# Kernel optimization log

Measured on AMD Instinct MI355X. Metric: run time of the kernel, lower is better.

## Reference

```python
import jax, jax.numpy as jnp
import numpy as np

H_DIM = 64      # input_dim of edge_aggregation (== h_dim)
HID = 128       # hidden_size of each per-edge-type agg MLP
T = 5           # edge_types for non-nba dataset
B, E, N = 64, 1024, 512


def setup_inputs() -> dict:
    key = jax.random.key(0)
    ks = jax.random.split(key, 8)
    edge_distribution = jax.random.uniform(ks[0], (B, E, T), dtype=jnp.float32)
    H = jax.random.uniform(ks[1], (B, E, N), dtype=jnp.float32)
    ori = jax.random.normal(ks[2], (B, N, H_DIM), dtype=jnp.float32)
    s1 = 1.0 / np.sqrt(H_DIM)
    s2 = 1.0 / np.sqrt(HID)
    # stacked per-edge-type MLP params: Linear(64->128) -> ReLU -> Linear(128->64)
    W1 = jax.random.uniform(ks[3], (T, H_DIM, HID), minval=-s1, maxval=s1, dtype=jnp.float32)
    b1 = jax.random.uniform(ks[4], (T, HID), minval=-s1, maxval=s1, dtype=jnp.float32)
    W2 = jax.random.uniform(ks[5], (T, HID, H_DIM), minval=-s2, maxval=s2, dtype=jnp.float32)
    b2 = jax.random.uniform(ks[6], (T, H_DIM), minval=-s2, maxval=s2, dtype=jnp.float32)
    return {"edge_distribution": edge_distribution, "H": H, "ori": ori,
            "W1": W1, "b1": b1, "W2": W2, "b2": b2}


def reference(edge_distribution, H, ori, W1, b1, W2, b2):
    # incidence gather: hyperedge features [B, E, D]
    edges = jnp.matmul(H, ori)
    # per-edge-type 2-layer MLP, vectorized over the T edge types
    h = jax.nn.relu(jnp.einsum('bed,tdh->bteh', edges, W1) + b1[None, :, None, :])
    per_type = jnp.einsum('bteh,thd->bted', h, W2) + b2[None, :, None, :]
    # mixture-weighted sum over edge types -> [B, E, D]
    edge_feature = jnp.einsum('bet,bted->bed', edge_distribution, per_type)
    # scatter back through H^T and concat with original node features
    node_agg = jnp.einsum('ben,bed->bnd', H, edge_feature)  # H^T @ edge_feature
    node_feature = jnp.concatenate((node_agg, ori), axis=-1)  # [B, N, 2D]
    return node_feature
```

## Files before the change

### kernel.cpp

```cpp
#include <hip/hip_runtime.h>

#define B_   64
#define E_   1024
#define N_   512
#define D_   64
#define HID_ 128
#define T_   5

typedef __bf16 bf16x8 __attribute__((ext_vector_type(8)));
typedef float f32x4 __attribute__((ext_vector_type(4)));

__device__ __forceinline__ unsigned short f2bu(float f) {
    union { float f; unsigned int u; } v; v.f = f;
    unsigned int r = (v.u + 0x7fffu + ((v.u >> 16) & 1u)) >> 16;
    return (unsigned short)r;
}

#define MFMA16(a, b, c) __builtin_amdgcn_mfma_f32_16x16x32_bf16((a), (b), (c), 0, 0, 0)

__global__ __launch_bounds__(256) void k_prep_w(const float* __restrict__ W1,
                                                const float* __restrict__ W2,
                                                unsigned short* __restrict__ W1T,
                                                unsigned short* __restrict__ W2T) {
    int idx = blockIdx.x * 256 + threadIdx.x;
    if (idx < T_ * HID_ * D_) {
        int t = idx / (HID_ * D_), rem = idx % (HID_ * D_);
        int h = rem / D_, d = rem % D_;
        W1T[idx] = f2bu(W1[(t * D_ + d) * HID_ + h]);
    } else {
        int j = idx - T_ * HID_ * D_;
        int t = j / (D_ * HID_), rem = j % (D_ * HID_);
        int d = rem / HID_, h = rem % HID_;
        W2T[j] = f2bu(W2[(t * HID_ + h) * D_ + d]);
    }
}

__global__ __launch_bounds__(256) void k_ori_prep(const float* __restrict__ ori,
                                                  float* __restrict__ out,
                                                  unsigned short* __restrict__ oriT) {
    int b = blockIdx.y, n0 = blockIdx.x * 64;
    __shared__ float tl[64 * 65];
    int tid = threadIdx.x;
    int dl = tid & 63;
    #pragma unroll 4
    for (int p = 0; p < 16; ++p) {
        int nn = p * 4 + (tid >> 6);
        float v = ori[(size_t)(b * N_ + n0 + nn) * D_ + dl];
        out[(size_t)(b * N_ + n0 + nn) * 128 + 64 + dl] = v;
        tl[dl * 65 + nn] = v;
    }
    __syncthreads();
    #pragma unroll 4
    for (int p = 0; p < 16; ++p) {
        int dd = p * 4 + (tid >> 6);
        oriT[(size_t)(b * D_ + dd) * N_ + n0 + dl] = f2bu(tl[dd * 65 + dl]);
    }
}

__global__ __launch_bounds__(256) void k_gemm_edges(const float* __restrict__ H,
                                                    const unsigned short* __restrict__ oriT,
                                                    unsigned short* __restrict__ edges) {
    int b = blockIdx.y, e0 = blockIdx.x * 128;
    __shared__ __align__(16) unsigned short aA[128 * 40];
    __shared__ __align__(16) unsigned short bB[64 * 40];
    int tid = threadIdx.x, w = tid >> 6, l = tid & 63, q = l >> 4, c = l & 15;
    const f32x4 zero = {0.f, 0.f, 0.f, 0.f};
    f32x4 acc[2][4];
    #pragma unroll
    for (int fm = 0; fm < 2; ++fm)
        #pragma unroll
        for (int fn = 0; fn < 4; ++fn) acc[fm][fn] = zero;

    for (int ks = 0; ks < 16; ++ks) {
        int k0 = ks * 32;
        #pragma unroll
        for (int p = 0; p < 4; ++p) {
            int u = p * 256 + tid, r = u >> 3, sg = u & 7;
            const float4 f = *(const float4*)&H[(size_t)(b * E_ + e0 + r) * N_ + k0 + sg * 4];
            ushort4 o;
            o.x = f2bu(f.x); o.y = f2bu(f.y); o.z = f2bu(f.z); o.w = f2bu(f.w);
            *(ushort4*)&aA[r * 40 + sg * 4] = o;
        }
        {
            int dd = tid >> 2, sg = tid & 3;
            *(uint4*)&bB[dd * 40 + sg * 8] =
                *(const uint4*)&oriT[(size_t)(b * D_ + dd) * N_ + k0 + sg * 8];
        }
        __syncthreads();
        bf16x8 a0 = *(const bf16x8*)&aA[(w * 32 + c) * 40 + q * 8];
        bf16x8 a1 = *(const bf16x8*)&aA[(w * 32 + 16 + c) * 40 + q * 8];
        #pragma unroll
        for (int fn = 0; fn < 4; ++fn) {
            bf16x8 bb = *(const bf16x8*)&bB[(fn * 16 + c) * 40 + q * 8];
            acc[0][fn] = MFMA16(a0, bb, acc[0][fn]);
            acc[1][fn] = MFMA16(a1, bb, acc[1][fn]);
        }
        __syncthreads();
    }
    #pragma unroll
    for (int fm = 0; fm < 2; ++fm)
        #pragma unroll
        for (int fn = 0; fn < 4; ++fn)
            #pragma unroll
            for (int i = 0; i < 4; ++i) {
                int e = e0 + w * 32 + fm * 16 + q * 4 + i;
                int d = fn * 16 + c;
                edges[(size_t)(b * E_ + e) * D_ + d] = f2bu(acc[fm][fn][i]);
            }
}

__global__ __launch_bounds__(256) void k_mlp(const unsigned short* __restrict__ edges,
                                             const float* __restrict__ ed,
                                             const float* __restrict__ b1,
                                             const float* __restrict__ b2,
                                             const unsigned short* __restrict__ W1T,
                                             const unsigned short* __restrict__ W2T,
                                             unsigned short* __restrict__ efT) {
    int bx = blockIdx.x;
    int b = bx >> 4, e0 = (bx & 15) * 64;
    __shared__ __align__(16) unsigned short a_sh[64 * 72];
    __shared__ __align__(16) unsigned short w_sh[128 * 72];
    __shared__ __align__(16) unsigned short h_sh[64 * 136];
    __shared__ float wd_sh[320];
    __shared__ float b1_sh[640];
    __shared__ float b2_sh[320];
    int tid = threadIdx.x, w = tid >> 6, l = tid & 63, q = l >> 4, c = l & 15;

    #pragma unroll
    for (int p = 0; p < 2; ++p) {
        int u = p * 256 + tid, r = u >> 3, sg = u & 7;
        *(uint4*)&a_sh[r * 72 + sg * 8] =
            *(const uint4*)&edges[(size_t)(b * E_ + e0 + r) * D_ + sg * 8];
    }
    for (int u = tid; u < 320; u += 256) wd_sh[u] = ed[(size_t)(b * E_ + e0) * T_ + u];
    for (int u = tid; u < 640; u += 256) b1_sh[u] = b1[u];
    for (int u = tid; u < 320; u += 256) b2_sh[u] = b2[u];

    const f32x4 zero = {0.f, 0.f, 0.f, 0.f};
    f32x4 y[4];
    #pragma unroll
    for (int fn = 0; fn < 4; ++fn) y[fn] = zero;

    for (int t = 0; t < T_; ++t) {
        __syncthreads();
        #pragma unroll
        for (int p = 0; p < 4; ++p) {
            int u = p * 256 + tid, hh = u >> 3, sg = u & 7;
            *(uint4*)&w_sh[hh * 72 + sg * 8] =
                *(const uint4*)&W1T[(t * HID_ + hh) * D_ + sg * 8];
        }
        __syncthreads();
        f32x4 hc[8];
        #pragma unroll
        for (int fn = 0; fn < 8; ++fn) hc[fn] = zero;
        #pragma unroll
        for (int ks = 0; ks < 2; ++ks) {
            bf16x8 a = *(const bf16x8*)&a_sh[(w * 16 + c) * 72 + ks * 32 + q * 8];
            #pragma unroll
            for (int fn = 0; fn < 8; ++fn) {
                bf16x8 bb = *(const bf16x8*)&w_sh[(fn * 16 + c) * 72 + ks * 32 + q * 8];
                hc[fn] = MFMA16(a, bb, hc[fn]);
            }
        }
        float wv[4];
        #pragma unroll
        for (int i = 0; i < 4; ++i) wv[i] = wd_sh[(w * 16 + q * 4 + i) * T_ + t];
        #pragma unroll
        for (int fn = 0; fn < 8; ++fn) {
            float b1v = b1_sh[t * HID_ + fn * 16 + c];
            #pragma unroll
            for (int i = 0; i < 4; ++i) {
                float v = hc[fn][i] + b1v;
                v = fmaxf(v, 0.0f) * wv[i];
                h_sh[(w * 16 + q * 4 + i) * 136 + fn * 16 + c] = f2bu(v);
            }
        }
        __syncthreads();
        #pragma unroll
        for (int p = 0; p < 4; ++p) {
            int u = p * 256 + tid, dd = u >> 4, sg = u & 15;
            *(uint4*)&w_sh[dd * 136 + sg * 8] =
                *(const uint4*)&W2T[(t * D_ + dd) * HID_ + sg * 8];
        }
        __syncthreads();
        #pragma unroll
        for (int ks = 0; ks < 4; ++ks) {
            bf16x8 a = *(const bf16x8*)&h_sh[(w * 16 + c) * 136 + ks * 32 + q * 8];
            #pragma unroll
            for (int fn = 0; fn < 4; ++fn) {
                bf16x8 bb = *(const bf16x8*)&w_sh[(fn * 16 + c) * 136 + ks * 32 + q * 8];
                y[fn] = MFMA16(a, bb, y[fn]);
            }
        }
    }
    #pragma unroll
    for (int fn = 0; fn < 4; ++fn) {
        int d = fn * 16 + c;
        ushort4 o;
        #pragma unroll
        for (int i = 0; i < 4; ++i) {
            int r = w * 16 + q * 4 + i;
            float s = y[fn][i];
            #pragma unroll
            for (int t = 0; t < T_; ++t) s += wd_sh[r * T_ + t] * b2_sh[t * D_ + d];
            ((unsigned short*)&o)[i] = f2bu(s);
        }
        *(ushort4*)&efT[(size_t)(b * D_ + d) * E_ + e0 + w * 16 + q * 4] = o;
    }
}

__global__ __launch_bounds__(256) void k_gemm_out(const float* __restrict__ H,
                                                  const unsigned short* __restrict__ efT,
                                                  float* __restrict__ out) {
    int b = blockIdx.y, n0 = blockIdx.x * 128;
    __shared__ __align__(16) unsigned short aA[128 * 40];
    __shared__ __align__(16) unsigned short bB[64 * 40];
    int tid = threadIdx.x, w = tid >> 6, l = tid & 63, q = l >> 4, c = l & 15;
    const f32x4 zero = {0.f, 0.f, 0.f, 0.f};
    f32x4 acc[2][4];
    #pragma unroll
    for (int fm = 0; fm < 2; ++fm)
        #pragma unroll
        for (int fn = 0; fn < 4; ++fn) acc[fm][fn] = zero;

    for (int ks = 0; ks < 32; ++ks) {
        #pragma unroll
        for (int p = 0; p < 4; ++p) {
            int u = p * 256 + tid, ke = u >> 5, sg = u & 31;
            const float4 f = *(const float4*)&H[(size_t)(b * E_ + ks * 32 + ke) * N_ + n0 + sg * 4];
            aA[(sg * 4 + 0) * 40 + ke] = f2bu(f.x);
            aA[(sg * 4 + 1) * 40 + ke] = f2bu(f.y);
            aA[(sg * 4 + 2) * 40 + ke] = f2bu(f.z);
            aA[(sg * 4 + 3) * 40 + ke] = f2bu(f.w);
        }
        {
            int dd = tid >> 2, sg = tid & 3;
            *(uint4*)&bB[dd * 40 + sg * 8] =
                *(const uint4*)&efT[(size_t)(b * D_ + dd) * E_ + ks * 32 + sg * 8];
        }
        __syncthreads();
        bf16x8 a0 = *(const bf16x8*)&aA[(w * 32 + c) * 40 + q * 8];
        bf16x8 a1 = *(const bf16x8*)&aA[(w * 32 + 16 + c) * 40 + q * 8];
        #pragma unroll
        for (int fn = 0; fn < 4; ++fn) {
            bf16x8 bb = *(const bf16x8*)&bB[(fn * 16 + c) * 40 + q * 8];
            acc[0][fn] = MFMA16(a0, bb, acc[0][fn]);
            acc[1][fn] = MFMA16(a1, bb, acc[1][fn]);
        }
        __syncthreads();
    }
    #pragma unroll
    for (int fm = 0; fm < 2; ++fm)
        #pragma unroll
        for (int fn = 0; fn < 4; ++fn)
            #pragma unroll
            for (int i = 0; i < 4; ++i) {
                int n = n0 + w * 32 + fm * 16 + q * 4 + i;
                out[(size_t)(b * N_ + n) * 128 + fn * 16 + c] = acc[fm][fn][i];
            }
}

extern "C" void kernel_launch(void* const* d_in, const int* in_sizes, int n_in,
                              void* d_out, int out_size, void* d_ws, size_t ws_size,
                              hipStream_t stream) {
    const float* ed  = (const float*)d_in[0];
    const float* H   = (const float*)d_in[1];
    const float* ori = (const float*)d_in[2];
    const float* W1  = (const float*)d_in[3];
    const float* b1  = (const float*)d_in[4];
    const float* W2  = (const float*)d_in[5];
    const float* b2  = (const float*)d_in[6];
    float* out = (float*)d_out;

    char* ws = (char*)d_ws;
    unsigned short* oriT  = (unsigned short*)ws; ws += (size_t)B_ * D_ * N_ * 2;
    unsigned short* W1T   = (unsigned short*)ws; ws += (size_t)T_ * HID_ * D_ * 2;
    unsigned short* W2T   = (unsigned short*)ws; ws += (size_t)T_ * D_ * HID_ * 2;
    unsigned short* edges = (unsigned short*)ws; ws += (size_t)B_ * E_ * D_ * 2;
    unsigned short* efT   = (unsigned short*)ws; ws += (size_t)B_ * D_ * E_ * 2;

    hipLaunchKernelGGL(k_prep_w, dim3(320), dim3(256), 0, stream, W1, W2, W1T, W2T);
    hipLaunchKernelGGL(k_ori_prep, dim3(8, 64), dim3(256), 0, stream, ori, out, oriT);
    hipLaunchKernelGGL(k_gemm_edges, dim3(8, 64), dim3(256), 0, stream, H, oriT, edges);
    hipLaunchKernelGGL(k_mlp, dim3(1024), dim3(256), 0, stream, edges, ed, b1, b2, W1T, W2T, efT);
    hipLaunchKernelGGL(k_gemm_out, dim3(4, 64), dim3(256), 0, stream, H, efT, out);
}
```

Before: 316.6 us.

## Pre-convert H to bf16 plus a transposed copy, and retile both GEMMs

Adds a k_prep_H kernel that reads the fp32 H once and writes two bf16 copies: row-major Hbf and a transposed HbfT. Both GEMMs then load bf16 tiles directly with 16-byte copies. This drops the per-tile fp32-to-bf16 conversion and the scattered scalar LDS transpose stores in k_gemm_out. Both GEMMs move to 64-wide K tiles, and k_gemm_out uses 64-row N tiles with vectorised f32x4 output stores, doubling its grid. The cost is extra memory traffic and workspace from writing and re-reading two 64 MB bf16 copies of H, plus one more kernel launch.

```diff
diff --git a/kernel.cpp b/kernel.cpp
--- a/kernel.cpp
+++ b/kernel.cpp
@@ -57,12 +57,37 @@
     }
 }
 
-__global__ __launch_bounds__(256) void k_gemm_edges(const float* __restrict__ H,
+__global__ __launch_bounds__(256) void k_prep_H(const float* __restrict__ H,
+                                                unsigned short* __restrict__ Hbf,
+                                                unsigned short* __restrict__ HbfT) {
+    int e0 = blockIdx.x * 64, n0 = blockIdx.y * 64, b = blockIdx.z;
+    __shared__ __align__(16) unsigned short tl[64 * 72];
+    int tid = threadIdx.x, r = tid >> 2, cg = tid & 3;
+    const float* src = &H[((size_t)b * E_ + e0 + r) * N_ + n0 + cg * 16];
+    unsigned short v[16];
+    #pragma unroll
+    for (int m = 0; m < 4; ++m) {
+        float4 f = *(const float4*)&src[m * 4];
+        v[m * 4 + 0] = f2bu(f.x); v[m * 4 + 1] = f2bu(f.y);
+        v[m * 4 + 2] = f2bu(f.z); v[m * 4 + 3] = f2bu(f.w);
+    }
+    unsigned short* dst = &Hbf[((size_t)b * E_ + e0 + r) * N_ + n0 + cg * 16];
+    *(uint4*)&dst[0] = *(const uint4*)&v[0];
+    *(uint4*)&dst[8] = *(const uint4*)&v[8];
+    #pragma unroll
+    for (int m = 0; m < 16; ++m) tl[(cg * 16 + m) * 72 + r] = v[m];
+    __syncthreads();
+    unsigned short* dstT = &HbfT[((size_t)b * N_ + n0 + r) * E_ + e0 + cg * 16];
+    *(uint4*)&dstT[0] = *(const uint4*)&tl[r * 72 + cg * 16];
+    *(uint4*)&dstT[8] = *(const uint4*)&tl[r * 72 + cg * 16 + 8];
+}
+
+__global__ __launch_bounds__(256) void k_gemm_edges(const unsigned short* __restrict__ Hbf,
                                                     const unsigned short* __restrict__ oriT,
                                                     unsigned short* __restrict__ edges) {
     int b = blockIdx.y, e0 = blockIdx.x * 128;
-    __shared__ __align__(16) unsigned short aA[128 * 40];
-    __shared__ __align__(16) unsigned short bB[64 * 40];
+    __shared__ __align__(16) unsigned short aA[128 * 72];
+    __shared__ __align__(16) unsigned short bB[64 * 72];
     int tid = threadIdx.x, w = tid >> 6, l = tid & 63, q = l >> 4, c = l & 15;
     const f32x4 zero = {0.f, 0.f, 0.f, 0.f};
     f32x4 acc[2][4];
@@ -71,29 +96,31 @@
         #pragma unroll
         for (int fn = 0; fn < 4; ++fn) acc[fm][fn] = zero;
 
-    for (int ks = 0; ks < 16; ++ks) {
-        int k0 = ks * 32;
+    for (int ks = 0; ks < 8; ++ks) {
+        int k0 = ks * 64;
         #pragma unroll
         for (int p = 0; p < 4; ++p) {
             int u = p * 256 + tid, r = u >> 3, sg = u & 7;
-            const float4 f = *(const float4*)&H[(size_t)(b * E_ + e0 + r) * N_ + k0 + sg * 4];
-            ushort4 o;
-            o.x = f2bu(f.x); o.y = f2bu(f.y); o.z = f2bu(f.z); o.w = f2bu(f.w);
-            *(ushort4*)&aA[r * 40 + sg * 4] = o;
-        }
-        {
-            int dd = tid >> 2, sg = tid & 3;
-            *(uint4*)&bB[dd * 40 + sg * 8] =
-                *(const uint4*)&oriT[(size_t)(b * D_ + dd) * N_ + k0 + sg * 8];
-        }
-        __syncthreads();
-        bf16x8 a0 = *(const bf16x8*)&aA[(w * 32 + c) * 40 + q * 8];
-        bf16x8 a1 = *(const bf16x8*)&aA[(w * 32 + 16 + c) * 40 + q * 8];
-        #pragma unroll
-        for (int fn = 0; fn < 4; ++fn) {
-            bf16x8 bb = *(const bf16x8*)&bB[(fn * 16 + c) * 40 + q * 8];
-            acc[0][fn] = MFMA16(a0, bb, acc[0][fn]);
-            acc[1][fn] = MFMA16(a1, bb, acc[1][fn]);
+            *(uint4*)&aA[r * 72 + sg * 8] =
+                *(const uint4*)&Hbf[((size_t)b * E_ + e0 + r) * N_ + k0 + sg * 8];
+        }
+        #pragma unroll
+        for (int p = 0; p < 2; ++p) {
+            int u = p * 256 + tid, r = u >> 3, sg = u & 7;
+            *(uint4*)&bB[r * 72 + sg * 8] =
+                *(const uint4*)&oriT[((size_t)b * D_ + r) * N_ + k0 + sg * 8];
+        }
+        __syncthreads();
+        #pragma unroll
+        for (int h = 0; h < 2; ++h) {
+            bf16x8 a0 = *(const bf16x8*)&aA[(w * 32 + c) * 72 + h * 32 + q * 8];
+            bf16x8 a1 = *(const bf16x8*)&aA[(w * 32 + 16 + c) * 72 + h * 32 + q * 8];
+            #pragma unroll
+            for (int fn = 0; fn < 4; ++fn) {
+                bf16x8 bb = *(const bf16x8*)&bB[(fn * 16 + c) * 72 + h * 32 + q * 8];
+                acc[0][fn] = MFMA16(a0, bb, acc[0][fn]);
+                acc[1][fn] = MFMA16(a1, bb, acc[1][fn]);
+            }
         }
         __syncthreads();
     }
@@ -105,7 +132,7 @@
             for (int i = 0; i < 4; ++i) {
                 int e = e0 + w * 32 + fm * 16 + q * 4 + i;
                 int d = fn * 16 + c;
-                edges[(size_t)(b * E_ + e) * D_ + d] = f2bu(acc[fm][fn][i]);
+                edges[((size_t)b * E_ + e) * D_ + d] = f2bu(acc[fm][fn][i]);
             }
 }
 
@@ -130,9 +157,9 @@
     for (int p = 0; p < 2; ++p) {
         int u = p * 256 + tid, r = u >> 3, sg = u & 7;
         *(uint4*)&a_sh[r * 72 + sg * 8] =
-            *(const uint4*)&edges[(size_t)(b * E_ + e0 + r) * D_ + sg * 8];
-    }
-    for (int u = tid; u < 320; u += 256) wd_sh[u] = ed[(size_t)(b * E_ + e0) * T_ + u];
+            *(const uint4*)&edges[((size_t)b * E_ + e0 + r) * D_ + sg * 8];
+    }
+    for (int u = tid; u < 320; u += 256) wd_sh[u] = ed[((size_t)b * E_ + e0) * T_ + u];
     for (int u = tid; u < 640; u += 256) b1_sh[u] = b1[u];
     for (int u = tid; u < 320; u += 256) b2_sh[u] = b2[u];
 
@@ -205,59 +232,52 @@
             for (int t = 0; t < T_; ++t) s += wd_sh[r * T_ + t] * b2_sh[t * D_ + d];
             ((unsigned short*)&o)[i] = f2bu(s);
         }
-        *(ushort4*)&efT[(size_t)(b * D_ + d) * E_ + e0 + w * 16 + q * 4] = o;
-    }
-}
-
-__global__ __launch_bounds__(256) void k_gemm_out(const float* __restrict__ H,
+        *(ushort4*)&efT[((size_t)b * D_ + d) * E_ + e0 + w * 16 + q * 4] = o;
+    }
+}
+
+__global__ __launch_bounds__(256) void k_gemm_out(const unsigned short* __restrict__ HbfT,
                                                   const unsigned short* __restrict__ efT,
                                                   float* __restrict__ out) {
-    int b = blockIdx.y, n0 = blockIdx.x * 128;
-    __shared__ __align__(16) unsigned short aA[128 * 40];
-    __shared__ __align__(16) unsigned short bB[64 * 40];
+    int b = blockIdx.y, n0 = blockIdx.x * 64;
+    __shared__ __align__(16) unsigned short aA[64 * 72];
+    __shared__ __align__(16) unsigned short bB[64 * 72];
     int tid = threadIdx.x, w = tid >> 6, l = tid & 63, q = l >> 4, c = l & 15;
     const f32x4 zero = {0.f, 0.f, 0.f, 0.f};
-    f32x4 acc[2][4];
-    #pragma unroll
-    for (int fm = 0; fm < 2; ++fm)
-        #pragma unroll
-        for (int fn = 0; fn < 4; ++fn) acc[fm][fn] = zero;
-
-    for (int ks = 0; ks < 32; ++ks) {
-        #pragma unroll
-        for (int p = 0; p < 4; ++p) {
-            int u = p * 256 + tid, ke = u >> 5, sg = u & 31;
-            const float4 f = *(const float4*)&H[(size_t)(b * E_ + ks * 32 + ke) * N_ + n0 + sg * 4];
-            aA[(sg * 4 + 0) * 40 + ke] = f2bu(f.x);
-            aA[(sg * 4 + 1) * 40 + ke] = f2bu(f.y);
-            aA[(sg * 4 + 2) * 40 + ke] = f2bu(f.z);
-            aA[(sg * 4 + 3) * 40 + ke] = f2bu(f.w);
-        }
-        {
-            int dd = tid >> 2, sg = tid & 3;
-            *(uint4*)&bB[dd * 40 + sg * 8] =
-                *(const uint4*)&efT[(size_t)(b * D_ + dd) * E_ + ks * 32 + sg * 8];
-        }
-        __syncthreads();
-        bf16x8 a0 = *(const bf16x8*)&aA[(w * 32 + c) * 40 + q * 8];
-        bf16x8 a1 = *(const bf16x8*)&aA[(w * 32 + 16 + c) * 40 + q * 8];
-        #pragma unroll
-        for (int fn = 0; fn < 4; ++fn) {
-            bf16x8 bb = *(const bf16x8*)&bB[(fn * 16 + c) * 40 + q * 8];
-            acc[0][fn] = MFMA16(a0, bb, acc[0][fn]);
-            acc[1][fn] = MFMA16(a1, bb, acc[1][fn]);
-        }
-        __syncthreads();
-    }
-    #pragma unroll
-    for (int fm = 0; fm < 2; ++fm)
-        #pragma unroll
-        for (int fn = 0; fn < 4; ++fn)
-            #pragma unroll
-            for (int i = 0; i < 4; ++i) {
-                int n = n0 + w * 32 + fm * 16 + q * 4 + i;
-                out[(size_t)(b * N_ + n) * 128 + fn * 16 + c] = acc[fm][fn][i];
-            }
+    f32x4 acc[4];
+    #pragma unroll
+    for (int fm = 0; fm < 4; ++fm) acc[fm] = zero;
+
+    for (int ks = 0; ks < 16; ++ks) {
+        int k0 = ks * 64;
+        #pragma unroll
+        for (int p = 0; p < 2; ++p) {
+            int u = p * 256 + tid, r = u >> 3, sg = u & 7;
+            *(uint4*)&aA[r * 72 + sg * 8] =
+                *(const uint4*)&efT[((size_t)b * D_ + r) * E_ + k0 + sg * 8];
+        }
+        #pragma unroll
+        for (int p = 0; p < 2; ++p) {
+            int u = p * 256 + tid, r = u >> 3, sg = u & 7;
+            *(uint4*)&bB[r * 72 + sg * 8] =
+                *(const uint4*)&HbfT[((size_t)b * N_ + n0 + r) * E_ + k0 + sg * 8];
+        }
+        __syncthreads();
+        #pragma unroll
+        for (int h = 0; h < 2; ++h) {
+            bf16x8 bfr = *(const bf16x8*)&bB[(w * 16 + c) * 72 + h * 32 + q * 8];
+            #pragma unroll
+            for (int fm = 0; fm < 4; ++fm) {
+                bf16x8 afr = *(const bf16x8*)&aA[(fm * 16 + c) * 72 + h * 32 + q * 8];
+                acc[fm] = MFMA16(afr, bfr, acc[fm]);
+            }
+        }
+        __syncthreads();
+    }
+    #pragma unroll
+    for (int fm = 0; fm < 4; ++fm) {
+        *(f32x4*)&out[((size_t)b * N_ + n0 + w * 16 + c) * 128 + fm * 16 + q * 4] = acc[fm];
+    }
 }
 
 extern "C" void kernel_launch(void* const* d_in, const int* in_sizes, int n_in,
@@ -278,10 +298,13 @@
     unsigned short* W2T   = (unsigned short*)ws; ws += (size_t)T_ * D_ * HID_ * 2;
     unsigned short* edges = (unsigned short*)ws; ws += (size_t)B_ * E_ * D_ * 2;
     unsigned short* efT   = (unsigned short*)ws; ws += (size_t)B_ * D_ * E_ * 2;
+    unsigned short* Hbf   = (unsigned short*)ws; ws += (size_t)B_ * E_ * N_ * 2;
+    unsigned short* HbfT  = (unsigned short*)ws; ws += (size_t)B_ * N_ * E_ * 2;
 
     hipLaunchKernelGGL(k_prep_w, dim3(320), dim3(256), 0, stream, W1, W2, W1T, W2T);
     hipLaunchKernelGGL(k_ori_prep, dim3(8, 64), dim3(256), 0, stream, ori, out, oriT);
-    hipLaunchKernelGGL(k_gemm_edges, dim3(8, 64), dim3(256), 0, stream, H, oriT, edges);
+    hipLaunchKernelGGL(k_prep_H, dim3(16, 8, 64), dim3(256), 0, stream, H, Hbf, HbfT);
+    hipLaunchKernelGGL(k_gemm_edges, dim3(8, 64), dim3(256), 0, stream, Hbf, oriT, edges);
     hipLaunchKernelGGL(k_mlp, dim3(1024), dim3(256), 0, stream, edges, ed, b1, b2, W1T, W2T, efT);
-    hipLaunchKernelGGL(k_gemm_out, dim3(4, 64), dim3(256), 0, stream, H, efT, out);
-}
+    hipLaunchKernelGGL(k_gemm_out, dim3(8, 64), dim3(256), 0, stream, HbfT, efT, out);
+}
```

Result: slower. 357.8 us (+13.0%).
